# Optimization experiments

Measured on AMD Instinct MI355X. Metric: run time of the kernel, lower is better.

## Reference

```python
import jax, jax.numpy as jnp
import numpy as np

B, C, H, W, R = 8, 256, 64, 64, 16


def setup_inputs() -> dict:
    key = jax.random.key(0)
    ks = jax.random.split(key, 14)
    def w(k, shape, fan):
        return (jax.random.normal(k, shape, jnp.float32) / np.sqrt(fan)).astype(jnp.float32)
    return {
        "features_depth": jax.random.normal(ks[0], (B, C, H, W), jnp.float32),
        "features_semseg": jax.random.normal(ks[1], (B, C, H, W), jnp.float32),
        "W0": w(ks[2], (C, 2 * C), 2 * C),          # conv_split0 1x1, [out,in]
        "Wdw": w(ks[3], (C, 1, 3, 3), 9),            # depthwise 3x3, groups=C
        "Wq": w(ks[4], (C, C), C),                   # Linear weights [out,in]
        "Wk": w(ks[5], (C, C), C),
        "Wv": w(ks[6], (C, C), C),
        "Wp": w(ks[7], (C, C), C),
        "bp": jnp.zeros((C,), jnp.float32),
        "Wsplit": w(ks[8], (C, C), C),               # conv_split 1x1
        "se_d_w1": w(ks[9], (C // R, C), C),         # SE squeeze conv1x1 (depth)
        "se_d_w2": w(ks[10], (C, C // R), C // R),
        "se_s_w1": w(ks[11], (C // R, C), C),        # SE squeeze conv1x1 (semseg)
        "se_s_w2": w(ks[12], (C, C // R), C // R),
    }


def _l2norm(a, eps=1e-12):
    n = jnp.linalg.norm(a, axis=-1, keepdims=True)
    return a / jnp.maximum(n, eps)


def _se(x, w1, w2):
    # x: [B,C,H,W]; global avg pool -> 1x1 convs -> sigmoid gate
    p = x.mean(axis=(2, 3))                                  # [B,C]
    h = jax.nn.relu(jnp.einsum('rc,bc->br', w1, p))          # [B,C/R]
    g = jax.nn.sigmoid(jnp.einsum('cr,br->bc', w2, h))       # [B,C]
    return x * g[:, :, None, None]


def reference(features_depth, features_semseg, W0, Wdw, Wq, Wk, Wv, Wp, bp,
              Wsplit, se_d_w1, se_d_w2, se_s_w1, se_s_w2):
    x = jnp.concatenate([features_depth, features_semseg], axis=1)  # [B,2C,H,W]
    x = jnp.einsum('oc,bchw->bohw', W0, x)                          # 1x1 conv
    x = jax.lax.conv_general_dilated(
        x, Wdw, window_strides=(1, 1), padding='SAME',
        dimension_numbers=('NCHW', 'OIHW', 'NCHW'), feature_group_count=C)
    xt = x.transpose(0, 2, 3, 1).reshape(B, H * W, C)               # [B,N,C]
    q = (xt @ Wq.T).transpose(0, 2, 1)                              # [B,C,N]
    k = (xt @ Wk.T).transpose(0, 2, 1)
    v = (xt @ Wv.T).transpose(0, 2, 1)
    q = _l2norm(q)
    k = _l2norm(k)
    attn = jax.nn.softmax(jnp.einsum('bcn,bdn->bcd', k, q), axis=-1)  # [B,C,C]
    y = jnp.einsum('bcd,bdn->bcn', attn, v)                         # [B,C,N]
    y = y.transpose(0, 2, 1)                                        # [B,N,C]
    y = y @ Wp.T + bp                                               # proj
    out_c = y.reshape(B, H, W, C).transpose(0, 3, 1, 2)             # [B,C,H,W]
    out_c = jnp.einsum('oc,bchw->bohw', Wsplit, out_c)              # 1x1 conv
    out_depth = _se(out_c, se_d_w1, se_d_w2) + features_depth
    out_semseg = _se(out_c, se_s_w1, se_s_w2) + features_semseg
    return (out_depth, out_semseg)
```

## Files before the change

kernel.cpp:

```cpp
#include <hip/hip_runtime.h>
#include <cstdint>

#define DEVI __device__ __forceinline__

using fx4 = __attribute__((ext_vector_type(4))) float;
using bf8 = __attribute__((ext_vector_type(8))) __bf16;
using s8v = __attribute__((ext_vector_type(8))) short;
using s4v = __attribute__((ext_vector_type(4))) short;
typedef unsigned short u16;
typedef unsigned int u32;

DEVI float b2f(u16 u) { return __builtin_bit_cast(float, (u32)u << 16); }
DEVI u16 f2b(float f) {
  u32 u = __builtin_bit_cast(u32, f);
  return (u16)((u + 0x7fffu + ((u >> 16) & 1u)) >> 16);
}

#define GLOAD(g, l)                                                          \
  __builtin_amdgcn_global_load_lds(                                          \
      (const __attribute__((address_space(1))) unsigned int*)(g),            \
      (__attribute__((address_space(3))) unsigned int*)(l), 16, 0, 0)

__global__ __launch_bounds__(256) void prep(const float* __restrict__ W0,
                                            const float* __restrict__ Wq,
                                            const float* __restrict__ Wk,
                                            const float* __restrict__ Wv,
                                            const float* __restrict__ Wsp,
                                            const float* __restrict__ Wp,
                                            const float* __restrict__ bp,
                                            u16* __restrict__ w0b,
                                            u16* __restrict__ wqk2,
                                            u16* __restrict__ wvtb,
                                            u16* __restrict__ wcb,
                                            float* __restrict__ bcb) {
  __shared__ float row[256];
  __shared__ float red[4];
  const int y = blockIdx.y;
  const int t = threadIdx.x;
  if (y == 0) {
    const int i = blockIdx.x * 256 + t;
    if (i < 131072) w0b[i] = f2b(W0[i]);
  } else if (y == 1) {
    const int i = blockIdx.x * 256 + t;
    if (i < 262144) {
      const int r = i >> 9, c = i & 511;
      const float* src = (r < 256) ? Wq : Wk;
      wqk2[i] = f2b(src[((r & 255) << 8) + (c & 255)]);
    }
  } else if (y == 2) {
    const int i = blockIdx.x * 256 + t;
    if (i < 65536) {
      const int e = i >> 8, d = i & 255;
      wvtb[i] = f2b(Wv[d * 256 + e]);
    }
  } else {
    if (blockIdx.x >= 256) return;
    const int o = blockIdx.x;
    row[t] = Wsp[o * 256 + t];
    __syncthreads();
    float acc = 0.f;
    for (int c = 0; c < 256; ++c) acc += row[c] * Wp[c * 256 + t];
    wcb[o * 256 + t] = f2b(acc);
    float pb = row[t] * bp[t];
#pragma unroll
    for (int m = 32; m > 0; m >>= 1) pb += __shfl_xor(pb, m);
    if ((t & 63) == 0) red[t >> 6] = pb;
    __syncthreads();
    if (t == 0) bcb[o] = red[0] + red[1] + red[2] + red[3];
  }
}

__global__ __launch_bounds__(512) void conv0f(const float* __restrict__ fd,
                                              const float* __restrict__ fs,
                                              const u16* __restrict__ w0b,
                                              u16* __restrict__ x0) {
  __shared__ u16 tmp[64 * 132];
  __shared__ u16 ldsA[128 * 64];
  __shared__ u16 ldsB[256 * 64];
  const int b = blockIdx.y;
  const int bm = blockIdx.x * 128;
  const int t = threadIdx.x;
  const int wid = t >> 6, lane = t & 63;
  const int wm = wid >> 2, wn = wid & 3;
  fx4 acc[4][4] = {};
  for (int kt = 0; kt < 512; kt += 64) {
#pragma unroll
    for (int i = 0; i < 4; ++i) {
      const int r = i * 64 + (t >> 3);
      const int kq = (t & 7) ^ (r & 7);
      GLOAD(w0b + (long)r * 512 + kt + kq * 8, &ldsB[i * 4096 + wid * 512]);
    }
    const float* src = ((kt < 256) ? fd : fs) + ((long)b * 256 + (kt & 255)) * 4096L + bm;
#pragma unroll
    for (int p = 0; p < 4; ++p) {
      const int c = (t >> 5) + p * 16;
      const int n4 = (t & 31) * 4;
      const fx4 v = *(const fx4*)&src[(long)c * 4096 + n4];
      s4v pk;
#pragma unroll
      for (int j = 0; j < 4; ++j) pk[j] = (short)f2b(v[j]);
      *(s4v*)&tmp[c * 132 + n4] = pk;
    }
    __syncthreads();
#pragma unroll
    for (int pass = 0; pass < 2; ++pass) {
      const int n = t & 127;
      const int g = (t >> 7) + pass * 4;
      s8v pk;
#pragma unroll
      for (int j = 0; j < 8; ++j) pk[j] = (short)tmp[(g * 8 + j) * 132 + n];
      *(s8v*)&ldsA[n * 64 + ((g ^ (n & 7)) * 8)] = pk;
    }
    __syncthreads();
#pragma unroll
    for (int ko = 0; ko < 2; ++ko) {
      bf8 af[4], bfr[4];
      const int kq = ko * 4 + (lane >> 4);
#pragma unroll
      for (int f = 0; f < 4; ++f) {
        const int ar = wm * 64 + f * 16 + (lane & 15);
        af[f] = *(const bf8*)&ldsA[ar * 64 + ((kq ^ (ar & 7)) * 8)];
        const int br = wn * 64 + f * 16 + (lane & 15);
        bfr[f] = *(const bf8*)&ldsB[br * 64 + ((kq ^ (br & 7)) * 8)];
      }
#pragma unroll
      for (int fm = 0; fm < 4; ++fm)
#pragma unroll
        for (int fn = 0; fn < 4; ++fn)
          acc[fm][fn] = __builtin_amdgcn_mfma_f32_16x16x32_bf16(af[fm], bfr[fn], acc[fm][fn], 0, 0, 0);
    }
    __syncthreads();
  }
#pragma unroll
  for (int fm = 0; fm < 4; ++fm) {
    const int m0 = wm * 64 + fm * 16 + ((lane >> 4) << 2);
#pragma unroll
    for (int fn = 0; fn < 4; ++fn) {
      const int o = wn * 64 + fn * 16 + (lane & 15);
#pragma unroll
      for (int r = 0; r < 4; ++r)
        x0[((long)b << 20) + (long)(bm + m0 + r) * 256 + o] = f2b(acc[fm][fn][r]);
    }
  }
}

template <typename OT, int BIAS, int EPI>
__global__ __launch_bounds__(256) void gemm_nt(
    const u16* __restrict__ A, long sA, int lda,
    const u16* __restrict__ B, long sB, int ldb,
    OT* __restrict__ C, long sC, long sCs, int ldc,
    const float* __restrict__ bias, int Keff, int ksplit,
    const float* __restrict__ wqf, const float* __restrict__ wkf,
    float* __restrict__ dpart, float* __restrict__ poolpart) {
  __shared__ u16 ldsA[128 * 64];
  __shared__ u16 ldsB[128 * 64];
  const int z = blockIdx.z;
  const int bb = z / ksplit;
  const int ss = z - bb * ksplit;
  const int bm = blockIdx.x * 128;
  const int bn = blockIdx.y * 128;
  const u16* Ab = A + bb * sA + (long)ss * Keff + (long)bm * lda;
  const u16* Bb = B + bb * sB + (long)ss * Keff + (long)bn * ldb;
  const int tid = threadIdx.x;
  const int wid = tid >> 6;
  const int lane = tid & 63;
  const int wm = wid >> 1, wn = wid & 1;
  const int srow = tid >> 3;
  const int slot = tid & 7;

  fx4 acc[4][4] = {};
  for (int kt = 0; kt < Keff; kt += 64) {
#pragma unroll
    for (int i = 0; i < 4; ++i) {
      const int row = i * 32 + srow;
      const int kq = slot ^ (row & 7);
      GLOAD(Ab + (long)row * lda + kt + kq * 8, &ldsA[i * 2048 + wid * 512]);
      GLOAD(Bb + (long)row * ldb + kt + kq * 8, &ldsB[i * 2048 + wid * 512]);
    }
    __syncthreads();
#pragma unroll
    for (int ko = 0; ko < 2; ++ko) {
      bf8 af[4], bfr[4];
      const int kq = ko * 4 + (lane >> 4);
#pragma unroll
      for (int f = 0; f < 4; ++f) {
        const int ar = wm * 64 + f * 16 + (lane & 15);
        af[f] = *(const bf8*)&ldsA[ar * 64 + ((kq ^ (ar & 7)) * 8)];
        const int br = wn * 64 + f * 16 + (lane & 15);
        bfr[f] = *(const bf8*)&ldsB[br * 64 + ((kq ^ (br & 7)) * 8)];
      }
#pragma unroll
      for (int fm = 0; fm < 4; ++fm)
#pragma unroll
        for (int fn = 0; fn < 4; ++fn)
          acc[fm][fn] = __builtin_amdgcn_mfma_f32_16x16x32_bf16(af[fm], bfr[fn], acc[fm][fn], 0, 0, 0);
    }
    __syncthreads();
  }
  if constexpr (EPI == 1) {
    u16* S2b = (u16*)C + bb * sC;
    float dp[4][4];
#pragma unroll
    for (int fm = 0; fm < 4; ++fm)
#pragma unroll
      for (int r = 0; r < 4; ++r) dp[fm][r] = 0.f;
#pragma unroll
    for (int fm = 0; fm < 4; ++fm) {
      const int m0 = bm + wm * 64 + fm * 16 + ((lane >> 4) << 2);
#pragma unroll
      for (int fn = 0; fn < 4; ++fn) {
        const int n0 = bn + wn * 64 + fn * 16 + (lane & 15);
#pragma unroll
        for (int r = 0; r < 4; ++r) {
          const float v = acc[fm][fn][r];
          const int m = m0 + r;
          if (m < 256) {
            const u16 hi = f2b(v);
            S2b[(long)m * 512 + n0] = hi;
            S2b[(long)m * 512 + 256 + n0] = f2b(v - b2f(hi));
          }
          const float* wr = (m < 256) ? (wqf + (long)m * 256) : (wkf + (long)(m - 256) * 256);
          dp[fm][r] += v * wr[n0];
        }
      }
    }
#pragma unroll
    for (int fm = 0; fm < 4; ++fm)
#pragma unroll
      for (int r = 0; r < 4; ++r) {
        float s = dp[fm][r];
        s += __shfl_xor(s, 1); s += __shfl_xor(s, 2);
        s += __shfl_xor(s, 4); s += __shfl_xor(s, 8);
        if ((lane & 15) == 0) {
          const int m = bm + wm * 64 + fm * 16 + ((lane >> 4) << 2) + r;
          dpart[(long)(blockIdx.y * 2 + wn) * 4096 + bb * 512 + m] = s;
        }
      }
    return;
  }
  if constexpr (EPI == 4) {
    float* odp = (float*)C + bb * sC;
    float* osp = (float*)C + 8388608 + bb * sC;
    const float* fdp = wqf + bb * sC;
    const float* fsp = wkf + bb * sC;
#pragma unroll
    for (int fm = 0; fm < 4; ++fm) {
      const int m0 = bm + wm * 64 + fm * 16 + ((lane >> 4) << 2);
#pragma unroll
      for (int r = 0; r < 4; ++r) {
        const int m = m0 + r;
        const float bv = bias[m];
        const float g1 = dpart[bb * 256 + m];
        const float g2 = poolpart[bb * 256 + m];
        const long rowb = (long)m * ldc;
#pragma unroll
        for (int fn = 0; fn < 4; ++fn) {
          const int n0 = bn + wn * 64 + fn * 16 + (lane & 15);
          const float v = acc[fm][fn][r] + bv;
          odp[rowb + n0] = v * g1 + fdp[rowb + n0];
          osp[rowb + n0] = v * g2 + fsp[rowb + n0];
        }
      }
    }
    return;
  }
  OT* Cb = C + bb * sC + ss * sCs;
#pragma unroll
  for (int fm = 0; fm < 4; ++fm) {
    const int m0 = bm + wm * 64 + fm * 16 + ((lane >> 4) << 2);
#pragma unroll
    for (int fn = 0; fn < 4; ++fn) {
      const int n0 = bn + wn * 64 + fn * 16 + (lane & 15);
#pragma unroll
      for (int r = 0; r < 4; ++r) {
        float v = acc[fm][fn][r];
        if (BIAS == 2) v += bias[m0 + r];
        if constexpr (sizeof(OT) == 2) Cb[(long)(m0 + r) * ldc + n0] = (OT)f2b(v);
        else Cb[(long)(m0 + r) * ldc + n0] = v;
      }
    }
  }
}

__global__ __launch_bounds__(256) void dwconvT(const u16* __restrict__ x,
                                               const float* __restrict__ wdw,
                                               u16* __restrict__ y,
                                               u16* __restrict__ yT,
                                               float* __restrict__ cspart) {
  __shared__ float w[9][256];
  __shared__ u16 tb2[32][264];
  __shared__ float psf[8][256];
  const int t = threadIdx.x;
  for (int i = t; i < 2304; i += 256) w[i % 9][i / 9] = wdw[i];
  const int b = blockIdx.x >> 7;
  const int strip = blockIdx.x & 127;
  const int n0 = strip * 32;
  const int h = n0 >> 6;
  const int w0 = n0 & 63;
  const int tc = (t & 31) * 8;
  const int tn = t >> 5;
  const u16* base = x + ((long)b << 20);
  float csl[8] = {0.f, 0.f, 0.f, 0.f, 0.f, 0.f, 0.f, 0.f};
  __syncthreads();
#pragma unroll
  for (int p = 0; p < 4; ++p) {
    const int nn = p * 8 + tn;
    const int ww = w0 + nn;
    float acc[8] = {0.f, 0.f, 0.f, 0.f, 0.f, 0.f, 0.f, 0.f};
#pragma unroll
    for (int ky = 0; ky < 3; ++ky) {
      const int hy = h + ky - 1;
      if ((unsigned)hy >= 64u) continue;
#pragma unroll
      for (int kx = 0; kx < 3; ++kx) {
        const int wx = ww + kx - 1;
        if ((unsigned)wx >= 64u) continue;
        const s8v v = *(const s8v*)&base[(((hy << 6) + wx) << 8) + tc];
        const int kk = ky * 3 + kx;
        const fx4 wa = *(const fx4*)&w[kk][tc];
        const fx4 wb = *(const fx4*)&w[kk][tc + 4];
#pragma unroll
        for (int j = 0; j < 4; ++j) {
          acc[j] += wa[j] * b2f((u16)v[j]);
          acc[4 + j] += wb[j] * b2f((u16)v[4 + j]);
        }
      }
    }
    s8v o;
#pragma unroll
    for (int j = 0; j < 8; ++j) {
      o[j] = (short)f2b(acc[j]);
      csl[j] += b2f((u16)o[j]);
    }
    *(s8v*)&y[((long)b << 20) + (long)((n0 + nn) << 8) + tc] = o;
    *(s8v*)&tb2[nn][tc] = o;
  }
#pragma unroll
  for (int j = 0; j < 8; ++j) psf[tn][tc + j] = csl[j];
  __syncthreads();
  const int cg = t >> 5;
  const int nn2 = t & 31;
  u16* yb = yT + ((long)b << 20);
#pragma unroll
  for (int cb = 0; cb < 256; cb += 8) {
    const int c = cb + cg;
    yb[(long)c * 4096 + n0 + nn2] = tb2[nn2][c];
  }
  if (t < 256) {
    float s = 0.f;
#pragma unroll
    for (int k = 0; k < 8; ++k) s += psf[k][t];
    cspart[(long)strip * 2048 + b * 256 + t] = s;
  }
}

__global__ __launch_bounds__(256) void gsplit(const float* __restrict__ part,
                                              u16* __restrict__ G2) {
  const int i4 = (blockIdx.x * 256 + threadIdx.x) * 4;
  fx4 s = {0.f, 0.f, 0.f, 0.f};
#pragma unroll
  for (int ss = 0; ss < 8; ++ss) s += *(const fx4*)(part + (long)ss * 524288 + i4);
  const int b = i4 >> 16, rem = i4 & 65535, e = rem >> 8, c0 = rem & 255;
  u16* d = G2 + (long)b * 131072 + (long)e * 512 + c0;
  s4v hi, lo;
#pragma unroll
  for (int j = 0; j < 4; ++j) {
    u16 h = f2b(s[j]);
    hi[j] = (short)h;
    lo[j] = (short)f2b(s[j] - b2f(h));
  }
  *(s4v*)d = hi;
  *(s4v*)(d + 256) = lo;
}

__global__ __launch_bounds__(256) void softmax_g2(const float* __restrict__ araw,
                                                  const float* __restrict__ dpart,
                                                  u16* __restrict__ out) {
  const int wid = threadIdx.x >> 6, lane = threadIdx.x & 63;
  const int t = threadIdx.x;
  const int b = blockIdx.x >> 6;
  __shared__ float rq[256];
  float dq = dpart[b * 512 + t] + dpart[4096 + b * 512 + t] +
             dpart[8192 + b * 512 + t] + dpart[12288 + b * 512 + t];
  rq[t] = 1.f / fmaxf(sqrtf(fmaxf(dq, 0.f)), 1e-12f);
  __syncthreads();
  const long row = (long)blockIdx.x * 4 + wid;
  const int c = (int)(row & 255);
  const int ki = b * 512 + 256 + c;
  float dk = dpart[ki] + dpart[4096 + ki] + dpart[8192 + ki] + dpart[12288 + ki];
  const float rk = 1.f / fmaxf(sqrtf(fmaxf(dk, 0.f)), 1e-12f);
  fx4 v = ((const fx4*)(araw + row * 256))[lane];
  v[0] *= rk * rq[lane * 4];     v[1] *= rk * rq[lane * 4 + 1];
  v[2] *= rk * rq[lane * 4 + 2]; v[3] *= rk * rq[lane * 4 + 3];
  float m = fmaxf(fmaxf(v[0], v[1]), fmaxf(v[2], v[3]));
#pragma unroll
  for (int o = 32; o > 0; o >>= 1) m = fmaxf(m, __shfl_xor(m, o));
  float e0 = __expf(v[0] - m), e1 = __expf(v[1] - m);
  float e2 = __expf(v[2] - m), e3 = __expf(v[3] - m);
  float s4 = e0 + e1 + e2 + e3;
#pragma unroll
  for (int o = 32; o > 0; o >>= 1) s4 += __shfl_xor(s4, o);
  const float inv = 1.f / s4;
  u16* op = out + row * 256 + lane * 4;
  op[0] = f2b(e0 * inv); op[1] = f2b(e1 * inv);
  op[2] = f2b(e2 * inv); op[3] = f2b(e3 * inv);
}

__global__ __launch_bounds__(256) void mwfuse(const u16* __restrict__ attnb,
                                              const u16* __restrict__ wvtb,
                                              const u16* __restrict__ wcb,
                                              u16* __restrict__ wfin) {
  __shared__ u16 lds[25088];
  const int M1OFF = 0;
  const int A2OFF = 16896;
  const int B1OFF = 0;
  const int A1OFF = 16384;
  const int e0 = blockIdx.x * 64;
  const int b = blockIdx.y;
  const int t = threadIdx.x;
  const int wid = t >> 6, lane = t & 63;
  const int srow = t >> 3, slot = t & 7;
  const u16* attn = attnb + (long)b * 65536;

  fx4 acc[4][4] = {};
  for (int kt = 0; kt < 256; kt += 64) {
#pragma unroll
    for (int i = 0; i < 8; ++i) {
      const int row = i * 32 + srow;
      const int kq = slot ^ (row & 7);
      GLOAD(attn + (long)row * 256 + kt + kq * 8, &lds[B1OFF + i * 2048 + wid * 512]);
    }
#pragma unroll
    for (int i = 0; i < 2; ++i) {
      const int row = i * 32 + srow;
      const int kq = slot ^ (row & 7);
      GLOAD(wvtb + (long)(e0 + row) * 256 + kt + kq * 8, &lds[A1OFF + i * 2048 + wid * 512]);
    }
    __syncthreads();
#pragma unroll
    for (int ko = 0; ko < 2; ++ko) {
      bf8 af[4], bfr[4];
      const int kq = ko * 4 + (lane >> 4);
#pragma unroll
      for (int f = 0; f < 4; ++f) {
        const int ar = f * 16 + (lane & 15);
        af[f] = *(const bf8*)&lds[A1OFF + ar * 64 + ((kq ^ (ar & 7)) * 8)];
        const int br = wid * 64 + f * 16 + (lane & 15);
        bfr[f] = *(const bf8*)&lds[B1OFF + br * 64 + ((kq ^ (br & 7)) * 8)];
      }
#pragma unroll
      for (int fm = 0; fm < 4; ++fm)
#pragma unroll
        for (int fn = 0; fn < 4; ++fn)
          acc[fm][fn] = __builtin_amdgcn_mfma_f32_16x16x32_bf16(af[fm], bfr[fn], acc[fm][fn], 0, 0, 0);
    }
    __syncthreads();
  }
#pragma unroll
  for (int fm = 0; fm < 4; ++fm) {
    const int ep0 = fm * 16 + ((lane >> 4) << 2);
#pragma unroll
    for (int fn = 0; fn < 4; ++fn) {
      const int c = wid * 64 + fn * 16 + (lane & 15);
#pragma unroll
      for (int r = 0; r < 4; ++r)
        lds[M1OFF + (ep0 + r) * 264 + c] = f2b(acc[fm][fn][r]);
    }
  }
  __syncthreads();
  fx4 acc2[4][4] = {};
  for (int kt = 0; kt < 256; kt += 32) {
#pragma unroll
    for (int i = 0; i < 4; ++i) {
      const int row = i * 64 + (t >> 2);
      const int kq = (t & 3) ^ (row & 3);
      GLOAD(wcb + (long)row * 256 + kt + kq * 8, &lds[A2OFF + i * 2048 + wid * 512]);
    }
    __syncthreads();
    bf8 af[4], bfr[4];
    const int kq = lane >> 4;
#pragma unroll
    for (int f = 0; f < 4; ++f) {
      const int ar = wid * 64 + f * 16 + (lane & 15);
      af[f] = *(const bf8*)&lds[A2OFF + ar * 32 + ((kq ^ (ar & 3)) * 8)];
      const int br = f * 16 + (lane & 15);
      bfr[f] = *(const bf8*)&lds[M1OFF + br * 264 + kt + kq * 8];
    }
#pragma unroll
    for (int fm = 0; fm < 4; ++fm)
#pragma unroll
      for (int fn = 0; fn < 4; ++fn)
        acc2[fm][fn] = __builtin_amdgcn_mfma_f32_16x16x32_bf16(af[fm], bfr[fn], acc2[fm][fn], 0, 0, 0);
    __syncthreads();
  }
  u16* wf = wfin + (long)b * 65536;
#pragma unroll
  for (int fm = 0; fm < 4; ++fm) {
    const int o0 = wid * 64 + fm * 16 + ((lane >> 4) << 2);
#pragma unroll
    for (int fn = 0; fn < 4; ++fn) {
      const int e = e0 + fn * 16 + (lane & 15);
#pragma unroll
      for (int r = 0; r < 4; ++r)
        wf[(long)(o0 + r) * 256 + e] = f2b(acc2[fm][fn][r]);
    }
  }
}

__global__ __launch_bounds__(256) void sefuse(const float* __restrict__ cspart,
                                              const u16* __restrict__ wfin,
                                              const float* __restrict__ bcb,
                                              const float* __restrict__ w1d, const float* __restrict__ w2d,
                                              const float* __restrict__ w1s, const float* __restrict__ w2s,
                                              float* __restrict__ gd, float* __restrict__ gs) {
  const int b = blockIdx.x;
  const int t = threadIdx.x;
  __shared__ float xm[256], p[256], hd[16], hs[16];
  float s = 0.f;
#pragma unroll 8
  for (int sl = 0; sl < 128; ++sl) s += cspart[(long)sl * 2048 + b * 256 + t];
  xm[t] = s;
  __syncthreads();
  const u16* wf = wfin + (long)b * 65536 + (long)t * 256;
  float acc = 0.f;
#pragma unroll 4
  for (int e = 0; e < 256; e += 8) {
    const s8v w8 = *(const s8v*)&wf[e];
    const fx4 x0v = *(const fx4*)&xm[e];
    const fx4 x1v = *(const fx4*)&xm[e + 4];
#pragma unroll
    for (int j = 0; j < 4; ++j) {
      acc += b2f((u16)w8[j]) * x0v[j];
      acc += b2f((u16)w8[4 + j]) * x1v[j];
    }
  }
  p[t] = acc * (1.f / 4096.f) + bcb[t];
  __syncthreads();
  if (t < 16) {
    float ad = 0.f, as2 = 0.f;
    for (int j = 0; j < 256; ++j) {
      ad += w1d[t * 256 + j] * p[j];
      as2 += w1s[t * 256 + j] * p[j];
    }
    hd[t] = fmaxf(ad, 0.f);
    hs[t] = fmaxf(as2, 0.f);
  }
  __syncthreads();
  float ad = 0.f, as2 = 0.f;
#pragma unroll
  for (int r = 0; r < 16; ++r) {
    ad += w2d[t * 16 + r] * hd[r];
    as2 += w2s[t * 16 + r] * hs[r];
  }
  gd[b * 256 + t] = 1.f / (1.f + __expf(-ad));
  gs[b * 256 + t] = 1.f / (1.f + __expf(-as2));
}

extern "C" void kernel_launch(void* const* d_in, const int* in_sizes, int n_in,
                              void* d_out, int out_size, void* d_ws, size_t ws_size,
                              hipStream_t stream) {
  const float* fd  = (const float*)d_in[0];
  const float* fs  = (const float*)d_in[1];
  const float* W0  = (const float*)d_in[2];
  const float* Wdw = (const float*)d_in[3];
  const float* Wq  = (const float*)d_in[4];
  const float* Wk  = (const float*)d_in[5];
  const float* Wv  = (const float*)d_in[6];
  const float* Wp  = (const float*)d_in[7];
  const float* bp  = (const float*)d_in[8];
  const float* Wsp = (const float*)d_in[9];
  const float* w1d = (const float*)d_in[10];
  const float* w2d = (const float*)d_in[11];
  const float* w1s = (const float*)d_in[12];
  const float* w2s = (const float*)d_in[13];

  char* ws = (char*)d_ws;
  u16* x0b    = (u16*)(ws + 0);
  u16* xtb    = (u16*)(ws + 16777216);
  u16* xtT    = (u16*)(ws + 33554432);
  float* part = (float*)(ws + 50331648);
  u16* G2     = (u16*)(ws + 67108864);
  u16* S2     = (u16*)(ws + 69206016);
  float* araw = (float*)(ws + 71303168);
  u16* attnb  = (u16*)(ws + 73400320);
  u16* wfin   = (u16*)(ws + 74448896);
  u16* w0b    = (u16*)(ws + 75497472);
  u16* wqk2   = (u16*)(ws + 75759616);
  u16* wvtb   = (u16*)(ws + 76283904);
  u16* wcb    = (u16*)(ws + 76414976);
  float* bcb  = (float*)(ws + 76546048);
  float* dpart = (float*)(ws + 76547072);
  float* cspart = (float*)(ws + 76611584);
  float* gdp  = (float*)(ws + 77660160);
  float* gsp  = (float*)(ws + 77668352);
  float* od   = (float*)d_out;

  prep<<<dim3(2048, 4), 256, 0, stream>>>(W0, Wq, Wk, Wv, Wsp, Wp, bp,
                                          w0b, wqk2, wvtb, wcb, bcb);
  conv0f<<<dim3(32, 8), 512, 0, stream>>>(fd, fs, w0b, x0b);
  dwconvT<<<1024, 256, 0, stream>>>(x0b, Wdw, xtb, xtT, cspart);
  gemm_nt<float, 0, 0><<<dim3(2, 2, 64), 256, 0, stream>>>(
      xtT, 1048576, 4096, xtT, 1048576, 4096,
      part, 65536, 524288, 256, nullptr, 512, 8, nullptr, nullptr, nullptr, nullptr);
  gsplit<<<512, 256, 0, stream>>>(part, G2);
  gemm_nt<u16, 0, 1><<<dim3(4, 2, 8), 256, 0, stream>>>(
      wqk2, 0, 512, G2, 131072, 512, S2, 131072, 0, 512, nullptr, 512, 1,
      Wq, Wk, dpart, nullptr);
  gemm_nt<float, 0, 0><<<dim3(2, 2, 8), 256, 0, stream>>>(
      wqk2 + 131072, 0, 512, S2, 131072, 512, araw, 65536, 0, 256, nullptr, 512, 1,
      nullptr, nullptr, nullptr, nullptr);
  softmax_g2<<<512, 256, 0, stream>>>(araw, dpart, attnb);
  mwfuse<<<dim3(4, 8), 256, 0, stream>>>(attnb, wvtb, wcb, wfin);
  sefuse<<<8, 256, 0, stream>>>(cspart, wfin, bcb, w1d, w2d, w1s, w2s, gdp, gsp);
  gemm_nt<float, 0, 4><<<dim3(2, 32, 8), 256, 0, stream>>>(
      wfin, 65536, 256, xtb, 1048576, 256, od, 1048576, 0, 4096, bcb, 256, 1,
      fd, fs, gdp, gsp);
}
```

Before: 165.8 us.

## Fuse attention-logit GEMM with L2-norm scaling and softmax into one kernel

```diff
diff --git a/kernel.cpp b/kernel.cpp
--- a/kernel.cpp
+++ b/kernel.cpp
@@ -373,37 +373,95 @@
   *(s4v*)(d + 256) = lo;
 }
 
-__global__ __launch_bounds__(256) void softmax_g2(const float* __restrict__ araw,
-                                                  const float* __restrict__ dpart,
-                                                  u16* __restrict__ out) {
-  const int wid = threadIdx.x >> 6, lane = threadIdx.x & 63;
+__global__ __launch_bounds__(256) void arawsm(const u16* __restrict__ wqk2,
+                                              const u16* __restrict__ S2,
+                                              const float* __restrict__ dpart,
+                                              u16* __restrict__ out) {
+  __shared__ u16 ldsA[128 * 64];
+  __shared__ u16 ldsB[256 * 64];
+  __shared__ float rqv[256];
+  __shared__ float rkv[128];
+  const int bm = blockIdx.x;
+  const int b  = blockIdx.y;
   const int t = threadIdx.x;
-  const int b = blockIdx.x >> 6;
-  __shared__ float rq[256];
-  float dq = dpart[b * 512 + t] + dpart[4096 + b * 512 + t] +
-             dpart[8192 + b * 512 + t] + dpart[12288 + b * 512 + t];
-  rq[t] = 1.f / fmaxf(sqrtf(fmaxf(dq, 0.f)), 1e-12f);
-  __syncthreads();
-  const long row = (long)blockIdx.x * 4 + wid;
-  const int c = (int)(row & 255);
-  const int ki = b * 512 + 256 + c;
-  float dk = dpart[ki] + dpart[4096 + ki] + dpart[8192 + ki] + dpart[12288 + ki];
-  const float rk = 1.f / fmaxf(sqrtf(fmaxf(dk, 0.f)), 1e-12f);
-  fx4 v = ((const fx4*)(araw + row * 256))[lane];
-  v[0] *= rk * rq[lane * 4];     v[1] *= rk * rq[lane * 4 + 1];
-  v[2] *= rk * rq[lane * 4 + 2]; v[3] *= rk * rq[lane * 4 + 3];
-  float m = fmaxf(fmaxf(v[0], v[1]), fmaxf(v[2], v[3]));
-#pragma unroll
-  for (int o = 32; o > 0; o >>= 1) m = fmaxf(m, __shfl_xor(m, o));
-  float e0 = __expf(v[0] - m), e1 = __expf(v[1] - m);
-  float e2 = __expf(v[2] - m), e3 = __expf(v[3] - m);
-  float s4 = e0 + e1 + e2 + e3;
-#pragma unroll
-  for (int o = 32; o > 0; o >>= 1) s4 += __shfl_xor(s4, o);
-  const float inv = 1.f / s4;
-  u16* op = out + row * 256 + lane * 4;
-  op[0] = f2b(e0 * inv); op[1] = f2b(e1 * inv);
-  op[2] = f2b(e2 * inv); op[3] = f2b(e3 * inv);
+  const int wid = t >> 6, lane = t & 63;
+  const int srow = t >> 3, slot = t & 7;
+  {
+    float dq = dpart[b * 512 + t] + dpart[4096 + b * 512 + t] +
+               dpart[8192 + b * 512 + t] + dpart[12288 + b * 512 + t];
+    rqv[t] = 1.f / fmaxf(sqrtf(fmaxf(dq, 0.f)), 1e-12f);
+    if (t < 128) {
+      const int ki = b * 512 + 256 + bm * 128 + t;
+      float dk = dpart[ki] + dpart[4096 + ki] + dpart[8192 + ki] + dpart[12288 + ki];
+      rkv[t] = 1.f / fmaxf(sqrtf(fmaxf(dk, 0.f)), 1e-12f);
+    }
+  }
+  const u16* Ab = wqk2 + 131072 + (long)(bm * 128) * 512;
+  const u16* Bb = S2 + (long)b * 131072;
+  fx4 acc[2][16] = {};
+  for (int kt = 0; kt < 512; kt += 64) {
+#pragma unroll
+    for (int i = 0; i < 4; ++i) {
+      const int row = i * 32 + srow;
+      const int kq = slot ^ (row & 7);
+      GLOAD(Ab + (long)row * 512 + kt + kq * 8, &ldsA[i * 2048 + wid * 512]);
+    }
+#pragma unroll
+    for (int i = 0; i < 8; ++i) {
+      const int row = i * 32 + srow;
+      const int kq = slot ^ (row & 7);
+      GLOAD(Bb + (long)row * 512 + kt + kq * 8, &ldsB[i * 2048 + wid * 512]);
+    }
+    __syncthreads();
+#pragma unroll
+    for (int ko = 0; ko < 2; ++ko) {
+      const int kq = ko * 4 + (lane >> 4);
+      const int ar0 = wid * 32 + (lane & 15);
+      const bf8 af0 = *(const bf8*)&ldsA[ar0 * 64 + ((kq ^ (ar0 & 7)) * 8)];
+      const int ar1 = wid * 32 + 16 + (lane & 15);
+      const bf8 af1 = *(const bf8*)&ldsA[ar1 * 64 + ((kq ^ (ar1 & 7)) * 8)];
+#pragma unroll
+      for (int fn = 0; fn < 16; ++fn) {
+        const int br = fn * 16 + (lane & 15);
+        const bf8 bfv = *(const bf8*)&ldsB[br * 64 + ((kq ^ (br & 7)) * 8)];
+        acc[0][fn] = __builtin_amdgcn_mfma_f32_16x16x32_bf16(af0, bfv, acc[0][fn], 0, 0, 0);
+        acc[1][fn] = __builtin_amdgcn_mfma_f32_16x16x32_bf16(af1, bfv, acc[1][fn], 0, 0, 0);
+      }
+    }
+    __syncthreads();
+  }
+  u16* outb = out + (long)b * 65536;
+  const int rq4 = lane >> 4;
+#pragma unroll
+  for (int mi = 0; mi < 2; ++mi) {
+#pragma unroll
+    for (int j = 0; j < 4; ++j) {
+      const int rlocal = wid * 32 + mi * 16 + rq4 * 4 + j;
+      const float rk = rkv[rlocal];
+      float v[16];
+      float mx = -3.4e38f;
+#pragma unroll
+      for (int fn = 0; fn < 16; ++fn) {
+        const int d = fn * 16 + (lane & 15);
+        v[fn] = acc[mi][fn][j] * rk * rqv[d];
+        mx = fmaxf(mx, v[fn]);
+      }
+      mx = fmaxf(mx, __shfl_xor(mx, 1));
+      mx = fmaxf(mx, __shfl_xor(mx, 2));
+      mx = fmaxf(mx, __shfl_xor(mx, 4));
+      mx = fmaxf(mx, __shfl_xor(mx, 8));
+      float s = 0.f;
+#pragma unroll
+      for (int fn = 0; fn < 16; ++fn) { v[fn] = __expf(v[fn] - mx); s += v[fn]; }
+      s += __shfl_xor(s, 1); s += __shfl_xor(s, 2);
+      s += __shfl_xor(s, 4); s += __shfl_xor(s, 8);
+      const float inv = 1.f / s;
+      const long rowb = (long)(bm * 128 + rlocal) * 256;
+#pragma unroll
+      for (int fn = 0; fn < 16; ++fn)
+        outb[rowb + fn * 16 + (lane & 15)] = f2b(v[fn] * inv);
+    }
+  }
 }
 
 __global__ __launch_bounds__(256) void mwfuse(const u16* __restrict__ attnb,
@@ -581,7 +639,6 @@
   float* part = (float*)(ws + 50331648);
   u16* G2     = (u16*)(ws + 67108864);
   u16* S2     = (u16*)(ws + 69206016);
-  float* araw = (float*)(ws + 71303168);
   u16* attnb  = (u16*)(ws + 73400320);
   u16* wfin   = (u16*)(ws + 74448896);
   u16* w0b    = (u16*)(ws + 75497472);
@@ -606,10 +663,7 @@
   gemm_nt<u16, 0, 1><<<dim3(4, 2, 8), 256, 0, stream>>>(
       wqk2, 0, 512, G2, 131072, 512, S2, 131072, 0, 512, nullptr, 512, 1,
       Wq, Wk, dpart, nullptr);
-  gemm_nt<float, 0, 0><<<dim3(2, 2, 8), 256, 0, stream>>>(
-      wqk2 + 131072, 0, 512, S2, 131072, 512, araw, 65536, 0, 256, nullptr, 512, 1,
-      nullptr, nullptr, nullptr, nullptr);
-  softmax_g2<<<512, 256, 0, stream>>>(araw, dpart, attnb);
+  arawsm<<<dim3(2, 8), 256, 0, stream>>>(wqk2, S2, dpart, attnb);
   mwfuse<<<dim3(4, 8), 256, 0, stream>>>(attnb, wvtb, wcb, wfin);
   sefuse<<<8, 256, 0, stream>>>(cspart, wfin, bcb, w1d, w2d, w1s, w2s, gdp, gsp);
   gemm_nt<float, 0, 4><<<dim3(2, 32, 8), 256, 0, stream>>>(
```

New measurement: 172.8 us. 4.2% more time.
